# Optimization experiments

Hardware: AMD Instinct MI355X
Metric: run time of the kernel (lower is better)

## Reference

```python
import jax, jax.numpy as jnp
from jax import lax
import numpy as np
import math

IN_SHAPE = [2, 4, 4]   # factorize(32, 4)
OUT_SHAPE = [2, 4, 4]
RANK = 8
GROUPS = 1
KH = KW = 3
OUT_CH = 32
IN_CH = 32


def setup_inputs() -> dict:
    key = jax.random.key(0)
    ks = jax.random.split(key, 6)

    def uni(k, shape, bound):
        return jax.random.uniform(k, shape, jnp.float32, -bound, bound)

    kernels = []
    for l in range(3):
        fi, fo = IN_SHAPE[l], OUT_SHAPE[l]
        bound = math.sqrt(6.0 / (fi + fo))
        kernels.append(uni(ks[l], (IN_SHAPE[l], OUT_SHAPE[l], RANK), bound))
    bound = math.sqrt(6.0 / (KH * KW * RANK + KH * KW))
    k3 = uni(ks[3], (GROUPS, KH, KW, RANK), bound)

    x = jax.random.normal(ks[4], (8, IN_CH, 512, 512), dtype=jnp.float32)
    bias = jnp.zeros((OUT_CH,), dtype=jnp.float32)
    return {"x": x, "k0": kernels[0], "k1": kernels[1], "k2": kernels[2],
            "k3": k3, "bias": bias}


def reference(x, k0, k1, k2, k3, bias):
    # CP weight reconstruction (chained einsums, as in the torch module)
    wl = jnp.einsum('iar,jbr->ijabr', k0, k1)          # [2,2,4,4,R]
    wr = jnp.einsum('kcr,ghwr->ghwkcr', k2, k3)        # [1,3,3,4,4,R]
    w = jnp.einsum('ijabr,ghwkcr->gijkabchw', wl, wr)  # [1,2,4,4,2,4,4,3,3]
    w = w.reshape(OUT_CH, IN_CH // GROUPS, KH, KW)     # [O, I, 3, 3]
    # flip + true convolution in conv_einsum == cross-correlation with w;
    # 'max'-mode output then [1:-1] trim == valid conv of the pad-1 input.
    out = lax.conv_general_dilated(
        x, w, window_strides=(1, 1), padding=((1, 1), (1, 1)),
        dimension_numbers=('NCHW', 'OIHW', 'NCHW'),
        feature_group_count=GROUPS)
    out = out + bias[None, :, None, None]
    return out  # [batch, out_channels, 512, 512]
```

## Files before the change

### kernel.cpp

```cpp
#include <hip/hip_runtime.h>
#include <hip/hip_bf16.h>

#define H 512
#define W 512
#define C 32
#define O 32
#define TW 64
#define TH 8

using bf16x8 = __attribute__((ext_vector_type(8))) short;
using f32x4  = __attribute__((ext_vector_type(4))) float;

__device__ __forceinline__ unsigned short f2bf(float f) {
    union { float f; unsigned u; } c; c.f = f;
    unsigned r = c.u + 0x7fffu + ((c.u >> 16) & 1u);
    return (unsigned short)(r >> 16);
}

__global__ void recon_w(const float* __restrict__ k0, const float* __restrict__ k1,
                        const float* __restrict__ k2, const float* __restrict__ k3,
                        unsigned short* __restrict__ wout) {
    int idx = blockIdx.x * 256 + threadIdx.x;
    if (idx >= 9 * 32 * 32) return;
    int ci = idx & 31;
    int o  = (idx >> 5) & 31;
    int s  = idx >> 10;
    int i = o >> 4, j = (o >> 2) & 3, k = o & 3;
    int a = ci >> 4, b = (ci >> 2) & 3, c = ci & 3;
    float acc = 0.f;
    #pragma unroll
    for (int r = 0; r < 8; ++r)
        acc += k0[(i*2 + a)*8 + r] * k1[(j*4 + b)*8 + r]
             * k2[(k*4 + c)*8 + r] * k3[s*8 + r];
    wout[idx] = f2bf(acc);
}

__launch_bounds__(256, 2)
__global__ void conv_mfma(const float* __restrict__ x,
                          const unsigned short* __restrict__ wq,
                          const float* __restrict__ bias,
                          float* __restrict__ out) {
    __shared__ __align__(16) unsigned short sx[TH + 2][TW + 2][C];

    const int tid = threadIdx.x;
    const int bid = blockIdx.x;
    const int n  = bid >> 9;
    const int r2 = bid & 511;
    const int ty = r2 >> 3;
    const int tx = r2 & 7;
    const int y0 = ty * TH, x0 = tx * TW;

    const int lane = tid & 63;
    const int pix  = lane & 15;
    const int quad = lane >> 4;

    bf16x8 bw[9][2];
    #pragma unroll
    for (int s = 0; s < 9; ++s)
        #pragma unroll
        for (int h = 0; h < 2; ++h)
            bw[s][h] = *(const bf16x8*)(wq + ((s*32 + h*16 + pix)*32 + quad*8));

    for (int task = tid; task < (TH + 2) * 4 * (TW + 2); task += 256) {
        int gxl = task % (TW + 2);
        int t2  = task / (TW + 2);
        int ciq = t2 & 3;
        int row = t2 >> 2;
        int gy = y0 + row - 1;
        int gx = x0 + gxl - 1;
        bool inb = (gy >= 0) && (gy < H) && (gx >= 0) && (gx < W);
        const float* p = x + (((n*C + ciq*8)*H + gy)*W + gx);
        float v[8];
        #pragma unroll
        for (int j2 = 0; j2 < 8; ++j2) v[j2] = inb ? p[j2 * H * W] : 0.f;
        uint4 pk;
        pk.x = (unsigned)f2bf(v[0]) | ((unsigned)f2bf(v[1]) << 16);
        pk.y = (unsigned)f2bf(v[2]) | ((unsigned)f2bf(v[3]) << 16);
        pk.z = (unsigned)f2bf(v[4]) | ((unsigned)f2bf(v[5]) << 16);
        pk.w = (unsigned)f2bf(v[6]) | ((unsigned)f2bf(v[7]) << 16);
        *(uint4*)&sx[row][gxl][ciq * 8] = pk;
    }
    __syncthreads();

    const int wave = tid >> 6;
    const float b0 = bias[pix];
    const float b1 = bias[16 + pix];

    for (int mt = 0; mt < 8; ++mt) {
        const int rr = mt >> 2;
        const int xm = (mt & 3) << 4;
        const int wrow = wave * 2 + rr;
        f32x4 acc0 = {0.f, 0.f, 0.f, 0.f};
        f32x4 acc1 = {0.f, 0.f, 0.f, 0.f};
        #pragma unroll
        for (int s = 0; s < 9; ++s) {
            const int dy = s / 3, dx = s % 3;
            bf16x8 a = *(const bf16x8*)&sx[wrow + dy][xm + pix + dx][quad * 8];
            acc0 = __builtin_amdgcn_mfma_f32_16x16x32_bf16(a, bw[s][0], acc0, 0, 0, 0);
            acc1 = __builtin_amdgcn_mfma_f32_16x16x32_bf16(a, bw[s][1], acc1, 0, 0, 0);
        }
        const int gy = y0 + wrow;
        const int base0 = ((n*O + pix)      * H + gy) * W + x0 + xm + quad * 4;
        const int base1 = ((n*O + 16 + pix) * H + gy) * W + x0 + xm + quad * 4;
        #pragma unroll
        for (int t = 0; t < 4; ++t) {
            out[base0 + t] = acc0[t] + b0;
            out[base1 + t] = acc1[t] + b1;
        }
    }
}

extern "C" void kernel_launch(void* const* d_in, const int* in_sizes, int n_in,
                              void* d_out, int out_size, void* d_ws, size_t ws_size,
                              hipStream_t stream) {
    const float* x    = (const float*)d_in[0];
    const float* k0   = (const float*)d_in[1];
    const float* k1   = (const float*)d_in[2];
    const float* k2   = (const float*)d_in[3];
    const float* k3   = (const float*)d_in[4];
    const float* bias = (const float*)d_in[5];
    float* out = (float*)d_out;
    unsigned short* wbuf = (unsigned short*)d_ws;

    recon_w<<<36, 256, 0, stream>>>(k0, k1, k2, k3, wbuf);
    conv_mfma<<<4096, 256, 0, stream>>>(x, wbuf, bias, out);
}
```

Measured before the change: 561.7 us.

## Pre-convert input to NHWC bf16 and run conv reading directly from global

Adds a separate pass that converts the NCHW fp32 input into an NHWC bf16 workspace buffer. A new conv kernel then loads MFMA operands straight from that buffer instead of staging a halo tile in shared memory, with boundary checks only on edge tiles and vectorized output stores. This trades an extra full read and write of the input, plus redundant global/L2 reads for the 3x3 taps, against removing the strided 8-plane gathers and LDS staging. It falls back to the old kernel when the workspace is too small.

```diff
diff --git a/kernel.cpp b/kernel.cpp
--- a/kernel.cpp
+++ b/kernel.cpp
@@ -5,8 +5,6 @@
 #define W 512
 #define C 32
 #define O 32
-#define TW 64
-#define TH 8
 
 using bf16x8 = __attribute__((ext_vector_type(8))) short;
 using f32x4  = __attribute__((ext_vector_type(4))) float;
@@ -35,13 +33,120 @@
     wout[idx] = f2bf(acc);
 }
 
+__global__ void nchw_to_nhwc(const float* __restrict__ x,
+                             unsigned short* __restrict__ xb) {
+    const int bid = blockIdx.x;
+    const int xs = bid & 1;
+    const int y  = (bid >> 1) & 511;
+    const int n  = bid >> 10;
+    const int tid = threadIdx.x;
+    const int cq = tid & 3;
+    const int pl = tid >> 2;
+    const int plane = H * W;
+    const float* src0 = x + (size_t)(n*C + cq*8) * plane + (size_t)y * W + xs * 256;
+    unsigned short* dst0 = xb + (((size_t)(n*H + y)) * W + xs * 256) * C + cq * 8;
+    #pragma unroll
+    for (int it = 0; it < 4; ++it) {
+        int px = it * 64 + pl;
+        float v[8];
+        #pragma unroll
+        for (int j = 0; j < 8; ++j) v[j] = src0[(size_t)j * plane + px];
+        uint4 pk;
+        pk.x = (unsigned)f2bf(v[0]) | ((unsigned)f2bf(v[1]) << 16);
+        pk.y = (unsigned)f2bf(v[2]) | ((unsigned)f2bf(v[3]) << 16);
+        pk.z = (unsigned)f2bf(v[4]) | ((unsigned)f2bf(v[5]) << 16);
+        pk.w = (unsigned)f2bf(v[6]) | ((unsigned)f2bf(v[7]) << 16);
+        *(uint4*)(dst0 + (size_t)px * C) = pk;
+    }
+}
+
+template<bool CHECK>
+__device__ __forceinline__ void do_mt(const unsigned short* __restrict__ nbase,
+                                      const int* rowoff, const int* syok,
+                                      int gx0, int pix, int quad,
+                                      const bf16x8 (&bw)[9][2],
+                                      float b0, float b1,
+                                      float* __restrict__ out, int orow0, int orow1) {
+    f32x4 acc0 = {b0, b0, b0, b0};
+    f32x4 acc1 = {b1, b1, b1, b1};
+    #pragma unroll
+    for (int dy = 0; dy < 3; ++dy) {
+        if (__builtin_amdgcn_readfirstlane(syok[dy])) {
+            const unsigned short* rp = nbase + rowoff[dy] + quad * 8;
+            #pragma unroll
+            for (int dx = 0; dx < 3; ++dx) {
+                int gx = gx0 + dx - 1 + pix;
+                bf16x8 a;
+                if (CHECK) {
+                    bf16x8 z = {0,0,0,0,0,0,0,0};
+                    a = ((unsigned)gx < (unsigned)W) ? *(const bf16x8*)(rp + gx*C) : z;
+                } else {
+                    a = *(const bf16x8*)(rp + gx*C);
+                }
+                acc0 = __builtin_amdgcn_mfma_f32_16x16x32_bf16(a, bw[dy*3+dx][0], acc0, 0, 0, 0);
+                acc1 = __builtin_amdgcn_mfma_f32_16x16x32_bf16(a, bw[dy*3+dx][1], acc1, 0, 0, 0);
+            }
+        }
+    }
+    const int ob = gx0 + quad * 4;
+    *(f32x4*)(out + orow0 + ob) = acc0;
+    *(f32x4*)(out + orow1 + ob) = acc1;
+}
+
+__launch_bounds__(256, 4)
+__global__ void conv_l1(const unsigned short* __restrict__ xb,
+                        const unsigned short* __restrict__ wq,
+                        const float* __restrict__ bias,
+                        float* __restrict__ out) {
+    const int tid = threadIdx.x;
+    const int bid = blockIdx.x;
+    const int xh = bid & 1;
+    const int yg = (bid >> 1) & 63;
+    const int n  = bid >> 7;
+    const int wave = tid >> 6;
+    const int lane = tid & 63;
+    const int pix = lane & 15, quad = lane >> 4;
+
+    bf16x8 bw[9][2];
+    #pragma unroll
+    for (int s = 0; s < 9; ++s)
+        #pragma unroll
+        for (int h = 0; h < 2; ++h)
+            bw[s][h] = *(const bf16x8*)(wq + ((s*32 + h*16 + pix)*32 + quad*8));
+
+    const float b0 = bias[pix];
+    const float b1 = bias[16 + pix];
+    const unsigned short* nbase = xb + (size_t)n * (H * W * C);
+    const int xbase = xh * 256;
+
+    for (int rr = 0; rr < 2; ++rr) {
+        const int gy = yg * 8 + wave * 2 + rr;
+        int rowoff[3], syok[3];
+        #pragma unroll
+        for (int dy = 0; dy < 3; ++dy) {
+            int sy = gy + dy - 1;
+            syok[dy] = ((unsigned)sy < (unsigned)H) ? 1 : 0;
+            rowoff[dy] = (syok[dy] ? sy : 0) * (W * C);
+        }
+        const int orow0 = ((n*O + pix) * H + gy) * W;
+        const int orow1 = orow0 + 16 * H * W;
+
+        do_mt<true >(nbase, rowoff, syok, xbase + 0,   pix, quad, bw, b0, b1, out, orow0, orow1);
+        #pragma unroll 2
+        for (int xm = 16; xm < 240; xm += 16)
+            do_mt<false>(nbase, rowoff, syok, xbase + xm, pix, quad, bw, b0, b1, out, orow0, orow1);
+        do_mt<true >(nbase, rowoff, syok, xbase + 240, pix, quad, bw, b0, b1, out, orow0, orow1);
+    }
+}
+
+#define TW 64
+#define TH 8
 __launch_bounds__(256, 2)
 __global__ void conv_mfma(const float* __restrict__ x,
                           const unsigned short* __restrict__ wq,
                           const float* __restrict__ bias,
                           float* __restrict__ out) {
     __shared__ __align__(16) unsigned short sx[TH + 2][TW + 2][C];
-
     const int tid = threadIdx.x;
     const int bid = blockIdx.x;
     const int n  = bid >> 9;
@@ -49,18 +154,15 @@
     const int ty = r2 >> 3;
     const int tx = r2 & 7;
     const int y0 = ty * TH, x0 = tx * TW;
-
     const int lane = tid & 63;
     const int pix  = lane & 15;
     const int quad = lane >> 4;
-
     bf16x8 bw[9][2];
     #pragma unroll
     for (int s = 0; s < 9; ++s)
         #pragma unroll
         for (int h = 0; h < 2; ++h)
             bw[s][h] = *(const bf16x8*)(wq + ((s*32 + h*16 + pix)*32 + quad*8));
-
     for (int task = tid; task < (TH + 2) * 4 * (TW + 2); task += 256) {
         int gxl = task % (TW + 2);
         int t2  = task / (TW + 2);
@@ -81,11 +183,9 @@
         *(uint4*)&sx[row][gxl][ciq * 8] = pk;
     }
     __syncthreads();
-
     const int wave = tid >> 6;
     const float b0 = bias[pix];
     const float b1 = bias[16 + pix];
-
     for (int mt = 0; mt < 8; ++mt) {
         const int rr = mt >> 2;
         const int xm = (mt & 3) << 4;
@@ -120,8 +220,17 @@
     const float* k3   = (const float*)d_in[4];
     const float* bias = (const float*)d_in[5];
     float* out = (float*)d_out;
-    unsigned short* wbuf = (unsigned short*)d_ws;
-
-    recon_w<<<36, 256, 0, stream>>>(k0, k1, k2, k3, wbuf);
-    conv_mfma<<<4096, 256, 0, stream>>>(x, wbuf, bias, out);
-}
+
+    unsigned short* wq = (unsigned short*)d_ws;
+    recon_w<<<36, 256, 0, stream>>>(k0, k1, k2, k3, wq);
+
+    const size_t xb_off  = 32768;
+    const size_t xb_size = (size_t)8 * H * W * C * 2;
+    if (ws_size >= xb_off + xb_size) {
+        unsigned short* xb = (unsigned short*)((char*)d_ws + xb_off);
+        nchw_to_nhwc<<<8 * H * 2 / 1, 256, 0, stream>>>(x, xb);
+        conv_l1<<<8 * 64 * 2, 256, 0, stream>>>(xb, wq, bias, out);
+    } else {
+        conv_mfma<<<4096, 256, 0, stream>>>(x, wq, bias, out);
+    }
+}
```

Result: slower. 708.1 us (+26.1%).
